# Kernel tuning notes

Hardware: AMD Instinct MI355X
Metric: run time of the kernel (lower is better)

## Reference

```python
import jax, jax.numpy as jnp
import numpy as np

N_NODES = 100000
N_EDGES = 1600000
N_FEAT, N_HID, N_CLS = 256, 64, 16


def setup_inputs() -> dict:
    key = jax.random.key(0)
    ks = jax.random.split(key, 8)
    x = jax.random.normal(ks[0], (N_NODES, N_FEAT), dtype=jnp.float32)
    adj_row = jax.random.randint(ks[1], (N_EDGES,), 0, N_NODES, dtype=jnp.int32)
    adj_col = jax.random.randint(ks[2], (N_EDGES,), 0, N_NODES, dtype=jnp.int32)
    adj_vals = jax.random.uniform(ks[3], (N_EDGES,), dtype=jnp.float32)
    W1 = jax.random.normal(ks[4], (N_FEAT, N_HID), dtype=jnp.float32) * 0.05
    b1 = jnp.zeros((N_HID,), dtype=jnp.float32)
    W2 = jax.random.normal(ks[5], (N_HID, N_CLS), dtype=jnp.float32) * 0.05
    b2 = jnp.zeros((N_CLS,), dtype=jnp.float32)
    return {"x": x, "adj_row": adj_row, "adj_col": adj_col, "adj_vals": adj_vals,
            "W1": W1, "b1": b1, "W2": W2, "b2": b2}


def _spmm(row, col, vals, h):
    # sparse [N,N] @ dense [N,D]: gather source rows, scale, scatter-add to dest rows
    msgs = vals[:, None] * h[col]                       # [E, D]
    return jax.ops.segment_sum(msgs, row, num_segments=N_NODES)


def reference(x, adj_row, adj_col, adj_vals, W1, b1, W2, b2):
    # layer 1: linear -> spmm -> relu  (dropout is identity at inference)
    h = _spmm(adj_row, adj_col, adj_vals, x @ W1 + b1)  # [N, n_hidden]
    h = jax.nn.relu(h)
    # layer 2: linear -> spmm -> log_softmax
    out = _spmm(adj_row, adj_col, adj_vals, h @ W2 + b2)  # [N, n_class]
    return jax.nn.log_softmax(out, axis=1)
```

## Files before the change

kernel.cpp:

```cpp
#include <hip/hip_runtime.h>

#define N_NODES 100000
#define N_EDGES 1600000
#define N_FEAT  256
#define N_HID   64
#define N_CLS   16
#define NB      391
#define CHUNK   8192
#define NSCAT   196
#define NGEMM1  1563

typedef unsigned short bfraw;
typedef unsigned int uint32;

typedef __attribute__((ext_vector_type(8))) short  bf16x8;
typedef __attribute__((ext_vector_type(4))) float  f32x4;

__device__ __forceinline__ bfraw f2bf(float f) {
    union { float f; unsigned int i; } v; v.f = f;
    unsigned int x = v.i;
    return (bfraw)((x + 0x7FFFu + ((x >> 16) & 1u)) >> 16);
}

__device__ __forceinline__ float bf_lo(uint32 g) { return __uint_as_float(g << 16); }
__device__ __forceinline__ float bf_hi(uint32 g) { return __uint_as_float(g & 0xFFFF0000u); }

__global__ __launch_bounds__(256) void w1cvt_hist_k(const float* __restrict__ W1,
                                                    bfraw* __restrict__ w1f,
                                                    const int* __restrict__ rowi,
                                                    int* __restrict__ bcnt) {
    __shared__ int lh[NB];
    if (blockIdx.x < 64) {
        int i = blockIdx.x * 256 + threadIdx.x;
        int k = i >> 6, n = i & 63;
        w1f[((size_t)((k >> 3) * 64 + n) << 3) + (k & 7)] = f2bf(W1[i]);
        return;
    }
    for (int i = threadIdx.x; i < NB; i += 256) lh[i] = 0;
    __syncthreads();
    const int4* r4p = (const int4*)rowi;
    for (int i = (blockIdx.x - 64) * 256 + threadIdx.x; i < N_EDGES / 4; i += 256 * 256) {
        int4 r = r4p[i];
        atomicAdd(&lh[r.x >> 8], 1);
        atomicAdd(&lh[r.y >> 8], 1);
        atomicAdd(&lh[r.z >> 8], 1);
        atomicAdd(&lh[r.w >> 8], 1);
    }
    __syncthreads();
    for (int i = threadIdx.x; i < NB; i += 256) {
        int c = lh[i];
        if (c) atomicAdd(&bcnt[i], c);
    }
}

__global__ __launch_bounds__(512) void bscan_k(const int* __restrict__ bcnt,
                                               int* __restrict__ bbase,
                                               int* __restrict__ gcur,
                                               int* __restrict__ rp) {
    __shared__ int s[512];
    int t = threadIdx.x;
    int v = (t < NB) ? bcnt[t] : 0;
    s[t] = v;
    __syncthreads();
    #pragma unroll
    for (int off = 1; off < 512; off <<= 1) {
        int x = (t >= off) ? s[t - off] : 0;
        __syncthreads();
        s[t] += x;
        __syncthreads();
    }
    if (t <= NB) {
        int b = s[t] - v;
        bbase[t] = b;
        if (t < NB) gcur[t] = b;
    }
    if (t == 0) rp[N_NODES] = N_EDGES;
}

__global__ __launch_bounds__(256) void scatter_gemm1_k(const int* __restrict__ rowi,
                                                       const int* __restrict__ coli,
                                                       const float* __restrict__ vals,
                                                       int* __restrict__ gcur,
                                                       int2* __restrict__ edges,
                                                       const float* __restrict__ x,
                                                       const bfraw* __restrict__ w1f,
                                                       const float* __restrict__ b1,
                                                       bfraw* __restrict__ h0) {
    __shared__ int lh[NB];
    __shared__ int lb[NB];
    const int t = threadIdx.x;

    if (blockIdx.x < NSCAT) {
        const int e0   = blockIdx.x * CHUNK;
        const bool full = (e0 + CHUNK <= N_EDGES);
        for (int i = t; i < NB; i += 256) lh[i] = 0;
        __syncthreads();

        int4 r4[8];
        if (full) {
            const int4* rp4 = (const int4*)(rowi + e0);
            #pragma unroll
            for (int u = 0; u < 8; ++u) r4[u] = rp4[t + u * 256];
            #pragma unroll
            for (int u = 0; u < 8; ++u) {
                atomicAdd(&lh[r4[u].x >> 8], 1);
                atomicAdd(&lh[r4[u].y >> 8], 1);
                atomicAdd(&lh[r4[u].z >> 8], 1);
                atomicAdd(&lh[r4[u].w >> 8], 1);
            }
        } else {
            for (int j = t; j < CHUNK; j += 256) {
                int e = e0 + j;
                if (e < N_EDGES) atomicAdd(&lh[rowi[e] >> 8], 1);
            }
        }
        __syncthreads();
        for (int i = t; i < NB; i += 256) {
            int c = lh[i];
            lb[i] = c ? atomicAdd(&gcur[i], c) : 0;
            lh[i] = 0;
        }
        __syncthreads();
        if (full) {
            const int4*   cp4 = (const int4*)(coli + e0);
            const float4* vp4 = (const float4*)(vals + e0);
            #pragma unroll
            for (int u = 0; u < 8; ++u) {
                int4   c4 = cp4[t + u * 256];
                float4 v4 = vp4[t + u * 256];
                int r, b, rk;
                r = r4[u].x; b = r >> 8; rk = atomicAdd(&lh[b], 1);
                edges[lb[b] + rk] = make_int2(c4.x | ((r & 255) << 17), __float_as_int(v4.x));
                r = r4[u].y; b = r >> 8; rk = atomicAdd(&lh[b], 1);
                edges[lb[b] + rk] = make_int2(c4.y | ((r & 255) << 17), __float_as_int(v4.y));
                r = r4[u].z; b = r >> 8; rk = atomicAdd(&lh[b], 1);
                edges[lb[b] + rk] = make_int2(c4.z | ((r & 255) << 17), __float_as_int(v4.z));
                r = r4[u].w; b = r >> 8; rk = atomicAdd(&lh[b], 1);
                edges[lb[b] + rk] = make_int2(c4.w | ((r & 255) << 17), __float_as_int(v4.w));
            }
        } else {
            for (int j = t; j < CHUNK; j += 256) {
                int e = e0 + j;
                if (e < N_EDGES) {
                    int r  = rowi[e];
                    int b  = r >> 8;
                    int rk = atomicAdd(&lh[b], 1);
                    edges[lb[b] + rk] = make_int2(coli[e] | ((r & 255) << 17),
                                                  __float_as_int(vals[e]));
                }
            }
        }
        return;
    }

    const int bg   = blockIdx.x - NSCAT;
    const int w    = t >> 6;
    const int lane = t & 63;
    const int q    = lane >> 4;
    const int m    = lane & 15;

    const int row  = bg * 64 + w * 16 + m;
    const int srow = row < N_NODES ? row : N_NODES - 1;
    const float* xp = x + (size_t)srow * N_FEAT + q * 8;
    const bf16x8* w1v = (const bf16x8*)w1f;

    f32x4 acc[4];
    #pragma unroll
    for (int nt = 0; nt < 4; ++nt) acc[nt] = (f32x4){0.f, 0.f, 0.f, 0.f};

    #pragma unroll
    for (int s = 0; s < 8; ++s) {
        float4 a0 = *(const float4*)(xp + s * 32);
        float4 a1 = *(const float4*)(xp + s * 32 + 4);
        bf16x8 af;
        af[0] = (short)f2bf(a0.x); af[1] = (short)f2bf(a0.y);
        af[2] = (short)f2bf(a0.z); af[3] = (short)f2bf(a0.w);
        af[4] = (short)f2bf(a1.x); af[5] = (short)f2bf(a1.y);
        af[6] = (short)f2bf(a1.z); af[7] = (short)f2bf(a1.w);
        const int g = s * 4 + q;
        #pragma unroll
        for (int nt = 0; nt < 4; ++nt) {
            bf16x8 bf_ = w1v[g * 64 + nt * 16 + m];
            acc[nt] = __builtin_amdgcn_mfma_f32_16x16x32_bf16(af, bf_, acc[nt], 0, 0, 0);
        }
    }

    float bb[4];
    #pragma unroll
    for (int nt = 0; nt < 4; ++nt) bb[nt] = b1[nt * 16 + m];

    const int orow0 = bg * 64 + w * 16 + q * 4;
    #pragma unroll
    for (int r = 0; r < 4; ++r) {
        int orow = orow0 + r;
        if (orow < N_NODES) {
            bfraw* op = h0 + (size_t)orow * N_HID + m;
            #pragma unroll
            for (int nt = 0; nt < 4; ++nt)
                op[nt * 16] = f2bf(acc[nt][r] + bb[nt]);
        }
    }
}

__global__ __launch_bounds__(256) void sort_k(const int* __restrict__ bbase,
                                              const int2* __restrict__ edges,
                                              int2* __restrict__ edges2,
                                              int* __restrict__ rp) {
    __shared__ int cnt[256];
    __shared__ int pos[256];
    const int t   = threadIdx.x;
    const int b   = blockIdx.x;
    const int beg = bbase[b];
    const int end = bbase[b + 1];

    cnt[t] = 0;
    __syncthreads();
    {
        int i = beg + t;
        for (; i + 768 < end; i += 1024) {
            int2 a = edges[i], c = edges[i + 256], d = edges[i + 512], e = edges[i + 768];
            atomicAdd(&cnt[(a.x >> 17) & 255], 1);
            atomicAdd(&cnt[(c.x >> 17) & 255], 1);
            atomicAdd(&cnt[(d.x >> 17) & 255], 1);
            atomicAdd(&cnt[(e.x >> 17) & 255], 1);
        }
        for (; i < end; i += 256)
            atomicAdd(&cnt[(edges[i].x >> 17) & 255], 1);
    }
    __syncthreads();

    int v = cnt[t];
    pos[t] = v;
    __syncthreads();
    #pragma unroll
    for (int off = 1; off < 256; off <<= 1) {
        int y = (t >= off) ? pos[t - off] : 0;
        __syncthreads();
        pos[t] += y;
        __syncthreads();
    }
    int excl = pos[t] - v;

    int row = (b << 8) + t;
    if (row < N_NODES) rp[row] = beg + excl;
    __syncthreads();
    pos[t] = excl;
    __syncthreads();

    {
        int i = beg + t;
        for (; i + 768 < end; i += 1024) {
            int2 E0 = edges[i], E1 = edges[i + 256], E2 = edges[i + 512], E3 = edges[i + 768];
            int r0 = (E0.x >> 17) & 255, r1 = (E1.x >> 17) & 255;
            int r2 = (E2.x >> 17) & 255, r3 = (E3.x >> 17) & 255;
            int k0 = atomicAdd(&pos[r0], 1);
            int k1 = atomicAdd(&pos[r1], 1);
            int k2 = atomicAdd(&pos[r2], 1);
            int k3 = atomicAdd(&pos[r3], 1);
            edges2[beg + k0] = make_int2(E0.x & 0x1FFFF, E0.y);
            edges2[beg + k1] = make_int2(E1.x & 0x1FFFF, E1.y);
            edges2[beg + k2] = make_int2(E2.x & 0x1FFFF, E2.y);
            edges2[beg + k3] = make_int2(E3.x & 0x1FFFF, E3.y);
        }
        for (; i < end; i += 256) {
            int2 E = edges[i];
            int r  = (E.x >> 17) & 255;
            int rk = atomicAdd(&pos[r], 1);
            edges2[beg + rk] = make_int2(E.x & 0x1FFFF, E.y);
        }
    }
}

__global__ __launch_bounds__(256) void spmm1_fused3_k(const int* __restrict__ rp,
                                                      const int2* __restrict__ edges2,
                                                      const uint32* __restrict__ h0p,
                                                      const float* __restrict__ W2,
                                                      const float* __restrict__ b2,
                                                      float* __restrict__ h2) {
    __shared__ float Hs[16][68];
    __shared__ float Ws[64 * 16];
    __shared__ float bs[16];
    const int t = threadIdx.x;
    *(float4*)&Ws[t * 4] = ((const float4*)W2)[t];
    if (t < 16) bs[t] = b2[t];

    const int g16 = t >> 4;
    const int l   = t & 15;
    const int row = blockIdx.x * 16 + g16;
    const int beg = rp[row];
    const int end = rp[row + 1];

    const uint2* h0v = (const uint2*)h0p;

    float a0 = 0.f, a1 = 0.f, a2 = 0.f, a3 = 0.f;
    int i = beg;
    for (; i + 8 <= end; i += 8) {
        int2 E[8];
        #pragma unroll
        for (int u = 0; u < 8; ++u) E[u] = edges2[i + u];
        uint2 q[8];
        #pragma unroll
        for (int u = 0; u < 8; ++u) q[u] = h0v[(size_t)E[u].x * 16 + l];
        #pragma unroll
        for (int u = 0; u < 8; ++u) {
            float v = __int_as_float(E[u].y);
            a0 += v * bf_lo(q[u].x); a1 += v * bf_hi(q[u].x);
            a2 += v * bf_lo(q[u].y); a3 += v * bf_hi(q[u].y);
        }
    }
    for (; i + 4 <= end; i += 4) {
        int2 E[4];
        #pragma unroll
        for (int u = 0; u < 4; ++u) E[u] = edges2[i + u];
        uint2 q[4];
        #pragma unroll
        for (int u = 0; u < 4; ++u) q[u] = h0v[(size_t)E[u].x * 16 + l];
        #pragma unroll
        for (int u = 0; u < 4; ++u) {
            float v = __int_as_float(E[u].y);
            a0 += v * bf_lo(q[u].x); a1 += v * bf_hi(q[u].x);
            a2 += v * bf_lo(q[u].y); a3 += v * bf_hi(q[u].y);
        }
    }
    for (; i < end; ++i) {
        int2 E = edges2[i];
        uint2 q = h0v[(size_t)E.x * 16 + l];
        float v = __int_as_float(E.y);
        a0 += v * bf_lo(q.x); a1 += v * bf_hi(q.x);
        a2 += v * bf_lo(q.y); a3 += v * bf_hi(q.y);
    }

    *(float4*)&Hs[g16][4 * l] = make_float4(fmaxf(a0, 0.f), fmaxf(a1, 0.f),
                                            fmaxf(a2, 0.f), fmaxf(a3, 0.f));
    __syncthreads();

    const int r = t >> 4;
    const int c = t & 15;
    float a = bs[c];
    #pragma unroll
    for (int k = 0; k < 64; ++k)
        a += Hs[r][k] * Ws[k * 16 + c];
    h2[(size_t)(blockIdx.x * 16 + r) * N_CLS + c] = a;
}

__global__ __launch_bounds__(256) void spmm2_lsm_k(const int* __restrict__ rp,
                                                   const int2* __restrict__ edges2,
                                                   const float* __restrict__ h2,
                                                   float* __restrict__ outp) {
    const int l   = threadIdx.x & 7;
    const int row = blockIdx.x * 32 + (threadIdx.x >> 3);
    const int beg = rp[row];
    const int end = rp[row + 1];
    const float2* h2v = (const float2*)h2;

    float a0 = 0.f, a1 = 0.f;
    int i = beg;
    for (; i + 4 <= end; i += 4) {
        int2 e0 = edges2[i + 0], e1 = edges2[i + 1];
        int2 e2 = edges2[i + 2], e3 = edges2[i + 3];
        float2 g0 = h2v[(size_t)e0.x * 8 + l];
        float2 g1 = h2v[(size_t)e1.x * 8 + l];
        float2 g2 = h2v[(size_t)e2.x * 8 + l];
        float2 g3 = h2v[(size_t)e3.x * 8 + l];
        float v0 = __int_as_float(e0.y), v1 = __int_as_float(e1.y);
        float v2 = __int_as_float(e2.y), v3 = __int_as_float(e3.y);
        a0 += v0 * g0.x; a1 += v0 * g0.y;
        a0 += v1 * g1.x; a1 += v1 * g1.y;
        a0 += v2 * g2.x; a1 += v2 * g2.y;
        a0 += v3 * g3.x; a1 += v3 * g3.y;
    }
    for (; i < end; ++i) {
        int2 e = edges2[i];
        float2 g = h2v[(size_t)e.x * 8 + l];
        float v = __int_as_float(e.y);
        a0 += v * g.x; a1 += v * g.y;
    }

    float m = fmaxf(a0, a1);
    #pragma unroll
    for (int off = 4; off; off >>= 1) m = fmaxf(m, __shfl_xor(m, off, 8));
    float ex = expf(a0 - m) + expf(a1 - m);
    float s = ex;
    #pragma unroll
    for (int off = 4; off; off >>= 1) s += __shfl_xor(s, off, 8);
    float ls = logf(s);
    *(float2*)(outp + (size_t)row * N_CLS + 2 * l) =
        make_float2(a0 - m - ls, a1 - m - ls);
}

extern "C" void kernel_launch(void* const* d_in, const int* in_sizes, int n_in,
                              void* d_out, int out_size, void* d_ws, size_t ws_size,
                              hipStream_t stream) {
    const float* x        = (const float*)d_in[0];
    const int*   adj_row  = (const int*)d_in[1];
    const int*   adj_col  = (const int*)d_in[2];
    const float* adj_vals = (const float*)d_in[3];
    const float* W1       = (const float*)d_in[4];
    const float* b1       = (const float*)d_in[5];
    const float* W2       = (const float*)d_in[6];
    const float* b2       = (const float*)d_in[7];
    float*       out      = (float*)d_out;

    const size_t H0_BYTES = (size_t)N_NODES * N_HID * sizeof(bfraw);
    const size_t H2_BYTES = (size_t)N_NODES * N_CLS * sizeof(float);
    const size_t E_BYTES  = (size_t)N_EDGES * sizeof(int2);
    bfraw* h0     = (bfraw*)d_ws;
    float* h2     = (float*)((char*)d_ws + H0_BYTES);
    int2*  edges  = (int2*)((char*)h2 + H2_BYTES);
    int2*  edges2 = (int2*)((char*)edges + E_BYTES);
    int*   bcnt   = (int*)((char*)edges2 + E_BYTES);
    int*   bbase  = bcnt + NB;
    int*   gcur   = bbase + NB + 1;
    int*   rp     = gcur + NB;
    bfraw* w1f    = (bfraw*)(rp + N_NODES + 1);

    hipMemsetAsync(bcnt, 0, NB * sizeof(int), stream);
    w1cvt_hist_k<<<320, 256, 0, stream>>>(W1, w1f, adj_row, bcnt);
    bscan_k<<<1, 512, 0, stream>>>(bcnt, bbase, gcur, rp);
    scatter_gemm1_k<<<NSCAT + NGEMM1, 256, 0, stream>>>(adj_row, adj_col, adj_vals,
                                                        gcur, edges,
                                                        x, w1f, b1, h0);
    sort_k<<<NB, 256, 0, stream>>>(bbase, edges, edges2, rp);

    spmm1_fused3_k<<<N_NODES / 16, 256, 0, stream>>>(rp, edges2, (const uint32*)h0,
                                                     W2, b2, h2);

    spmm2_lsm_k<<<N_NODES / 32, 256, 0, stream>>>(rp, edges2, h2, out);
}
```

Before: 283.2 us.

## Replace global histogram atomics with partials, prefetch GEMM rows, unroll spmm2 gathers

```diff
diff --git a/kernel.cpp b/kernel.cpp
--- a/kernel.cpp
+++ b/kernel.cpp
@@ -9,6 +9,7 @@
 #define CHUNK   8192
 #define NSCAT   196
 #define NGEMM1  1563
+#define NHIST   256
 
 typedef unsigned short bfraw;
 typedef unsigned int uint32;
@@ -28,7 +29,7 @@
 __global__ __launch_bounds__(256) void w1cvt_hist_k(const float* __restrict__ W1,
                                                     bfraw* __restrict__ w1f,
                                                     const int* __restrict__ rowi,
-                                                    int* __restrict__ bcnt) {
+                                                    int* __restrict__ part) {
     __shared__ int lh[NB];
     if (blockIdx.x < 64) {
         int i = blockIdx.x * 256 + threadIdx.x;
@@ -36,10 +37,11 @@
         w1f[((size_t)((k >> 3) * 64 + n) << 3) + (k & 7)] = f2bf(W1[i]);
         return;
     }
+    const int hb = blockIdx.x - 64;
     for (int i = threadIdx.x; i < NB; i += 256) lh[i] = 0;
     __syncthreads();
     const int4* r4p = (const int4*)rowi;
-    for (int i = (blockIdx.x - 64) * 256 + threadIdx.x; i < N_EDGES / 4; i += 256 * 256) {
+    for (int i = hb * 256 + threadIdx.x; i < N_EDGES / 4; i += 256 * 256) {
         int4 r = r4p[i];
         atomicAdd(&lh[r.x >> 8], 1);
         atomicAdd(&lh[r.y >> 8], 1);
@@ -47,19 +49,21 @@
         atomicAdd(&lh[r.w >> 8], 1);
     }
     __syncthreads();
-    for (int i = threadIdx.x; i < NB; i += 256) {
-        int c = lh[i];
-        if (c) atomicAdd(&bcnt[i], c);
-    }
-}
-
-__global__ __launch_bounds__(512) void bscan_k(const int* __restrict__ bcnt,
+    for (int i = threadIdx.x; i < NB; i += 256)
+        part[hb * NB + i] = lh[i];
+}
+
+__global__ __launch_bounds__(512) void bscan_k(const int* __restrict__ part,
                                                int* __restrict__ bbase,
                                                int* __restrict__ gcur,
                                                int* __restrict__ rp) {
     __shared__ int s[512];
     int t = threadIdx.x;
-    int v = (t < NB) ? bcnt[t] : 0;
+    int v = 0;
+    if (t < NB) {
+        #pragma unroll 8
+        for (int hb = 0; hb < NHIST; ++hb) v += part[hb * NB + t];
+    }
     s[t] = v;
     __syncthreads();
     #pragma unroll
@@ -164,19 +168,24 @@
     const float* xp = x + (size_t)srow * N_FEAT + q * 8;
     const bf16x8* w1v = (const bf16x8*)w1f;
 
+    float4 x0[8], x1[8];
+    #pragma unroll
+    for (int s = 0; s < 8; ++s) {
+        x0[s] = *(const float4*)(xp + s * 32);
+        x1[s] = *(const float4*)(xp + s * 32 + 4);
+    }
+
     f32x4 acc[4];
     #pragma unroll
     for (int nt = 0; nt < 4; ++nt) acc[nt] = (f32x4){0.f, 0.f, 0.f, 0.f};
 
     #pragma unroll
     for (int s = 0; s < 8; ++s) {
-        float4 a0 = *(const float4*)(xp + s * 32);
-        float4 a1 = *(const float4*)(xp + s * 32 + 4);
         bf16x8 af;
-        af[0] = (short)f2bf(a0.x); af[1] = (short)f2bf(a0.y);
-        af[2] = (short)f2bf(a0.z); af[3] = (short)f2bf(a0.w);
-        af[4] = (short)f2bf(a1.x); af[5] = (short)f2bf(a1.y);
-        af[6] = (short)f2bf(a1.z); af[7] = (short)f2bf(a1.w);
+        af[0] = (short)f2bf(x0[s].x); af[1] = (short)f2bf(x0[s].y);
+        af[2] = (short)f2bf(x0[s].z); af[3] = (short)f2bf(x0[s].w);
+        af[4] = (short)f2bf(x1[s].x); af[5] = (short)f2bf(x1[s].y);
+        af[6] = (short)f2bf(x1[s].z); af[7] = (short)f2bf(x1[s].w);
         const int g = s * 4 + q;
         #pragma unroll
         for (int nt = 0; nt < 4; ++nt) {
@@ -355,19 +364,31 @@
 
     float a0 = 0.f, a1 = 0.f;
     int i = beg;
+    for (; i + 8 <= end; i += 8) {
+        int2 e[8];
+        #pragma unroll
+        for (int u = 0; u < 8; ++u) e[u] = edges2[i + u];
+        float2 g[8];
+        #pragma unroll
+        for (int u = 0; u < 8; ++u) g[u] = h2v[(size_t)e[u].x * 8 + l];
+        #pragma unroll
+        for (int u = 0; u < 8; ++u) {
+            float v = __int_as_float(e[u].y);
+            a0 += v * g[u].x; a1 += v * g[u].y;
+        }
+    }
     for (; i + 4 <= end; i += 4) {
-        int2 e0 = edges2[i + 0], e1 = edges2[i + 1];
-        int2 e2 = edges2[i + 2], e3 = edges2[i + 3];
-        float2 g0 = h2v[(size_t)e0.x * 8 + l];
-        float2 g1 = h2v[(size_t)e1.x * 8 + l];
-        float2 g2 = h2v[(size_t)e2.x * 8 + l];
-        float2 g3 = h2v[(size_t)e3.x * 8 + l];
-        float v0 = __int_as_float(e0.y), v1 = __int_as_float(e1.y);
-        float v2 = __int_as_float(e2.y), v3 = __int_as_float(e3.y);
-        a0 += v0 * g0.x; a1 += v0 * g0.y;
-        a0 += v1 * g1.x; a1 += v1 * g1.y;
-        a0 += v2 * g2.x; a1 += v2 * g2.y;
-        a0 += v3 * g3.x; a1 += v3 * g3.y;
+        int2 e[4];
+        #pragma unroll
+        for (int u = 0; u < 4; ++u) e[u] = edges2[i + u];
+        float2 g[4];
+        #pragma unroll
+        for (int u = 0; u < 4; ++u) g[u] = h2v[(size_t)e[u].x * 8 + l];
+        #pragma unroll
+        for (int u = 0; u < 4; ++u) {
+            float v = __int_as_float(e[u].y);
+            a0 += v * g[u].x; a1 += v * g[u].y;
+        }
     }
     for (; i < end; ++i) {
         int2 e = edges2[i];
@@ -408,15 +429,14 @@
     float* h2     = (float*)((char*)d_ws + H0_BYTES);
     int2*  edges  = (int2*)((char*)h2 + H2_BYTES);
     int2*  edges2 = (int2*)((char*)edges + E_BYTES);
-    int*   bcnt   = (int*)((char*)edges2 + E_BYTES);
-    int*   bbase  = bcnt + NB;
+    int*   bbase  = (int*)((char*)edges2 + E_BYTES);
     int*   gcur   = bbase + NB + 1;
     int*   rp     = gcur + NB;
     bfraw* w1f    = (bfraw*)(rp + N_NODES + 1);
-
-    hipMemsetAsync(bcnt, 0, NB * sizeof(int), stream);
-    w1cvt_hist_k<<<320, 256, 0, stream>>>(W1, w1f, adj_row, bcnt);
-    bscan_k<<<1, 512, 0, stream>>>(bcnt, bbase, gcur, rp);
+    int*   part   = (int*)(w1f + 16384);
+
+    w1cvt_hist_k<<<320, 256, 0, stream>>>(W1, w1f, adj_row, part);
+    bscan_k<<<1, 512, 0, stream>>>(part, bbase, gcur, rp);
     scatter_gemm1_k<<<NSCAT + NGEMM1, 256, 0, stream>>>(adj_row, adj_col, adj_vals,
                                                         gcur, edges,
                                                         x, w1f, b1, h0);
```

New measurement: 280.6 us. Within noise of the previous version (-0.9%).
